# Kernel tuning notes

Measured on AMD Instinct MI355X. Metric: run time of the kernel, lower is better.

## Reference

```python
import jax, jax.numpy as jnp
import numpy as np


def setup_inputs() -> dict:
    key = jax.random.key(0)
    k1, k2 = jax.random.split(key)
    B, Nq, Nk, D = 8, 2048, 2048, 512
    query = jax.random.normal(k1, (B, Nq, D), dtype=jnp.float32)
    kv = jax.random.normal(k2, (B, Nk, D), dtype=jnp.float32)
    return {"query": query, "key": kv}


def reference(query, key):
    # Unscaled dot-product attention; value tensor is `key` itself.
    scores = jnp.einsum('bqd,bkd->bqk', query, key)  # [B, Nq, Nk]
    probs = jax.nn.softmax(scores, axis=-1)
    return jnp.einsum('bqk,bkd->bqd', probs, key)
```

## Files before the change

kernel.cpp:

```cpp
#include <hip/hip_runtime.h>

typedef _Float16 half8   __attribute__((ext_vector_type(8)));
typedef float    floatx4 __attribute__((ext_vector_type(4)));
typedef float    floatx16 __attribute__((ext_vector_type(16)));
typedef unsigned uintx2  __attribute__((ext_vector_type(2)));

#define LOG2E 1.44269504088896340736f

#define NQ  2048
#define NK  2048
#define DIM 512
#define KT  32
#define NTILES 64
#define IMG_BYTES 32768
#define WS_NEED ((size_t)8 * NTILES * IMG_BYTES)

#define PKRT(a,b) __builtin_bit_cast(unsigned, __builtin_amdgcn_cvt_pkrtz((a),(b)))


__global__ __launch_bounds__(256, 2)
void prep_k(const float* __restrict__ Kg, char* __restrict__ wsK)
{
    __shared__ __align__(16) _Float16 sImg[KT * DIM];
    const int tid = threadIdx.x;
    const int tileIdx = blockIdx.x;
    const int batch = tileIdx >> 6;
    const int kt    = tileIdx & 63;

    #pragma unroll
    for (int i = 0; i < 4; ++i) {
        const int idx = i * 256 + tid;
        const int k  = idx >> 5;
        const int db = idx & 31;
        const float* kp = Kg + ((size_t)batch * NK + (size_t)kt * KT + k) * DIM + db * 16;
        float4 f0 = *(const float4*)(kp + 0);
        float4 f1 = *(const float4*)(kp + 4);
        float4 f2 = *(const float4*)(kp + 8);
        float4 f3 = *(const float4*)(kp + 12);
        uint4 w0, w1;
        w0.x = PKRT(f0.x, f0.y); w0.y = PKRT(f0.z, f0.w);
        w0.z = PKRT(f1.x, f1.y); w0.w = PKRT(f1.z, f1.w);
        w1.x = PKRT(f2.x, f2.y); w1.y = PKRT(f2.z, f2.w);
        w1.z = PKRT(f3.x, f3.y); w1.w = PKRT(f3.z, f3.w);
        const int off = ((k >> 4) * 32 + db) * 256 + (k & 15) * 16;
        *(uint4*)&sImg[off + 0] = w0;
        *(uint4*)&sImg[off + 8] = w1;
    }
    __syncthreads();
    char* dst = wsK + (size_t)tileIdx * IMG_BYTES;
    const char* src = (const char*)sImg;
    #pragma unroll
    for (int i = 0; i < 8; ++i) {
        const int off = i * 4096 + tid * 16;
        *(uint4*)(dst + off) = *(const uint4*)(src + off);
    }
}

__device__ __forceinline__ void gld16(const char* g, char* l)
{
    __builtin_amdgcn_global_load_lds(
        (const __attribute__((address_space(1))) void*)g,
        (__attribute__((address_space(3))) void*)l, 16, 0, 0);
}

__global__ __launch_bounds__(512, 2)
void attn_fa3(const float* __restrict__ Qg, const char* __restrict__ wsK,
              float* __restrict__ Og)
{
    __shared__ __align__(16) char  sK[2][2][IMG_BYTES];
    __shared__ __align__(16) float sSx[8 * 64 * 8];

    const int tid  = threadIdx.x;
    const int lane = tid & 63;
    const int wave = tid >> 6;
    const int strip  = wave & 1;
    const int dh     = (wave >> 1) & 1;
    const int stream = wave >> 2;
    const int ql   = lane & 31;
    const int h    = lane >> 5;

    const int batch = blockIdx.x & 7;
    const int qtile = blockIdx.x >> 3;
    const int qrow  = qtile * 64 + strip * 32 + ql;
    const int dbase = dh * 256;

    const char* img = wsK + ((size_t)(batch * NTILES + stream * 32)) * IMG_BYTES;

    const float* qp = Qg + ((size_t)batch * NQ + qrow) * DIM + dbase + h * 8;
    half8 qf[16];
    #pragma unroll
    for (int dc = 0; dc < 16; ++dc) {
        float4 f0 = *(const float4*)(qp + dc * 16);
        float4 f1 = *(const float4*)(qp + dc * 16 + 4);
        union { unsigned u[4]; half8 hh; } t;
        t.u[0] = PKRT(f0.x, f0.y); t.u[1] = PKRT(f0.z, f0.w);
        t.u[2] = PKRT(f1.x, f1.y); t.u[3] = PKRT(f1.z, f1.w);
        qf[dc] = t.hh;
    }
    asm volatile("" ::: "memory");

    floatx16 acc[8];
    #pragma unroll
    for (int dt = 0; dt < 8; ++dt) {
        #pragma unroll
        for (int e = 0; e < 16; ++e) acc[dt][e] = 0.f;
    }
    float m_run = -INFINITY;
    float l_run = 0.f;

    const int laneA = ((lane >> 4) & 1) * 16384 + (lane & 15) * 32 + h * 16;
    const int laneT = ((lane >> 4) & 1) * 512 + h * 256 + (lane & 15) * 8;

    auto issue = [&](int t, int bi) {
        const char* src = img + (size_t)t * IMG_BYTES;
        char* dst = &sK[stream][bi][0];
        const int cw = (wave & 3) * 8;
        #pragma unroll
        for (int i = 0; i < 8; ++i) {
            const int c = cw + i;
            gld16(src + c * 1024 + lane * 16, dst + c * 1024);
        }
    };

    issue(0, 0);

    for (int kt = 0; kt < 32; ++kt) {
        const int bi = kt & 1;
        issue((kt + 1) & 31, bi ^ 1);

        asm volatile("s_waitcnt vmcnt(8)" ::: "memory");
        __builtin_amdgcn_s_barrier();
        __builtin_amdgcn_sched_barrier(0);

        const char* buf = &sK[stream][bi][0];

        union SS { floatx16 v; floatx4 q[4]; float f[16]; } s;
        {
            floatx16 sv;
            #pragma unroll
            for (int e = 0; e < 16; ++e) sv[e] = 0.f;
            const char* ap = buf + dh * 8192 + laneA;
            #pragma unroll
            for (int dc = 0; dc < 16; ++dc) {
                half8 a = *(const half8*)(ap + dc * 512);
                sv = __builtin_amdgcn_mfma_f32_32x32x16_f16(a, qf[dc], sv, 0, 0, 0);
            }
            s.v = sv;
        }

        float* slot  = &sSx[(wave * 64 + lane) * 8];
        const float* pslot = &sSx[((wave ^ 2) * 64 + lane) * 8];
        *(floatx4*)(slot + 0) = s.q[0];
        *(floatx4*)(slot + 4) = s.q[1];
        asm volatile("s_waitcnt lgkmcnt(0)" ::: "memory");
        __builtin_amdgcn_s_barrier();
        __builtin_amdgcn_sched_barrier(0);
        floatx4 r0 = *(const floatx4*)(pslot + 0);
        floatx4 r1 = *(const floatx4*)(pslot + 4);
        asm volatile("s_waitcnt lgkmcnt(0)" ::: "memory");
        __builtin_amdgcn_s_barrier();
        __builtin_amdgcn_sched_barrier(0);
        *(floatx4*)(slot + 0) = s.q[2];
        *(floatx4*)(slot + 4) = s.q[3];
        s.q[0] += r0; s.q[1] += r1;
        asm volatile("s_waitcnt lgkmcnt(0)" ::: "memory");
        __builtin_amdgcn_s_barrier();
        __builtin_amdgcn_sched_barrier(0);
        floatx4 r2 = *(const floatx4*)(pslot + 0);
        floatx4 r3 = *(const floatx4*)(pslot + 4);
        s.q[2] += r2; s.q[3] += r3;

        float mloc = s.f[0];
        #pragma unroll
        for (int r = 1; r < 16; ++r) mloc = fmaxf(mloc, s.f[r]);
        mloc = fmaxf(mloc, __shfl_xor(mloc, 32));
        const float m_new = fmaxf(m_run, mloc);
        const int grow = __any(mloc > m_run);

        float sl = 0.f;
        unsigned pk[8];
        #pragma unroll
        for (int s8 = 0; s8 < 8; ++s8) {
            const float pa = exp2f((s.f[2 * s8]     - m_new) * LOG2E);
            const float pb = exp2f((s.f[2 * s8 + 1] - m_new) * LOG2E);
            sl += pa + pb;
            pk[s8] = PKRT(pa, pb);
        }
        sl += __shfl_xor(sl, 32);
        if (grow) {
            const float alpha = exp2f((m_run - m_new) * LOG2E);
            l_run = l_run * alpha + sl;
            m_run = m_new;
            #pragma unroll
            for (int dt = 0; dt < 8; ++dt) acc[dt] *= alpha;
        } else {
            l_run += sl;
        }

        unsigned sw[8];
        #pragma unroll
        for (int s8 = 0; s8 < 8; ++s8)
            sw[s8] = (unsigned)__shfl_xor((int)pk[s8], 32);
        union PB { unsigned u[4]; half8 hh; } b0, b1;
        b0.u[0] = h ? sw[2] : pk[0];  b0.u[1] = h ? sw[3] : pk[1];
        b0.u[2] = h ? pk[2] : sw[0];  b0.u[3] = h ? pk[3] : sw[1];
        b1.u[0] = h ? sw[6] : pk[4];  b1.u[1] = h ? sw[7] : pk[5];
        b1.u[2] = h ? pk[6] : sw[4];  b1.u[3] = h ? pk[7] : sw[5];

        const unsigned bufA =
            (unsigned)(size_t)(__attribute__((address_space(3))) const char*)buf
            + (unsigned)(dh * 8192 + laneT);
        #pragma unroll
        for (int dt = 0; dt < 8; ++dt) {
            uintx2 t0, t1, t2, t3;
            const unsigned a0 = bufA + dt * 1024;
            const unsigned a1 = a0 + 16384;
            asm volatile(
                "ds_read_b64_tr_b16 %0, %4\n\t"
                "ds_read_b64_tr_b16 %1, %4 offset:128\n\t"
                "ds_read_b64_tr_b16 %2, %5\n\t"
                "ds_read_b64_tr_b16 %3, %5 offset:128"
                : "=&v"(t0), "=&v"(t1), "=&v"(t2), "=&v"(t3)
                : "v"(a0), "v"(a1));
            asm volatile("s_waitcnt lgkmcnt(0)" ::: "memory");
            __builtin_amdgcn_sched_barrier(0);
            union AF { uintx2 d[2]; half8 hh; } A0, A1;
            A0.d[0] = t0; A0.d[1] = t1;
            A1.d[0] = t2; A1.d[1] = t3;
            acc[dt] = __builtin_amdgcn_mfma_f32_32x32x16_f16(A0.hh, b0.hh, acc[dt], 0, 0, 0);
            acc[dt] = __builtin_amdgcn_mfma_f32_32x32x16_f16(A1.hh, b1.hh, acc[dt], 0, 0, 0);
        }

        __builtin_amdgcn_s_barrier();
        __builtin_amdgcn_sched_barrier(0);
    }

    {
        sSx[(wave * 64 + lane) * 2 + 0] = m_run;
        sSx[(wave * 64 + lane) * 2 + 1] = l_run;
        __syncthreads();
        const float pm = sSx[((wave ^ 4) * 64 + lane) * 2 + 0];
        const float pl = sSx[((wave ^ 4) * 64 + lane) * 2 + 1];
        const float mt   = fmaxf(m_run, pm);
        const float aown = exp2f((m_run - mt) * LOG2E);
        const float aoth = exp2f((pm   - mt) * LOG2E);
        const float lt   = l_run * aown + pl * aoth;
        const float inv  = 1.f / lt;
        (void)aoth;
        __syncthreads();

        float* op = Og + ((size_t)batch * NQ + qrow) * DIM + dbase;
        #pragma unroll
        for (int dt = 0; dt < 8; ++dt) {
            union SS2 { floatx16 v; floatx4 q[4]; } w;
            w.v = acc[dt] * aown;
            if (stream == 1) {
                float* sp = &sSx[(((wave & 3) * 64) + lane) * 16];
                *(floatx4*)(sp + 0)  = w.q[0];
                *(floatx4*)(sp + 4)  = w.q[1];
                *(floatx4*)(sp + 8)  = w.q[2];
                *(floatx4*)(sp + 12) = w.q[3];
            }
            __syncthreads();
            if (stream == 0) {
                const float* sp = &sSx[((wave * 64) + lane) * 16];
                #pragma unroll
                for (int g = 0; g < 4; ++g) {
                    floatx4 r = *(const floatx4*)(sp + g * 4);
                    floatx4 o = (w.q[g] + r) * inv;
                    *(floatx4*)(op + dt * 32 + g * 8 + 4 * h) = o;
                }
            }
            __syncthreads();
        }
    }
}

__global__ __launch_bounds__(256, 2)
void attn_fa(const float* __restrict__ Qg, const float* __restrict__ Kg,
             float* __restrict__ Og)
{
    __shared__ __align__(16) _Float16 sKr[KT * 512];
    __shared__ __align__(16) _Float16 sKt[256 * 72];
    __shared__ __align__(16) float    sSx[4 * 2 * 64 * 4];

    const int tid  = threadIdx.x;
    const int lane = tid & 63;
    const int wave = tid >> 6;
    const int quad = lane >> 4;
    const int col  = lane & 15;
    const int wq   = wave & 1;
    const int wg   = wave >> 1;
    const int dbase = wg * 256;

    const int batch = blockIdx.x & 7;
    const int qtile = blockIdx.x >> 3;
    const int qrow  = qtile * 32 + wq * 16 + col;

    const float* qp = Qg + ((size_t)batch * NQ + qrow) * DIM + dbase + quad * 8;
    half8 qf[8];
    #pragma unroll
    for (int dc = 0; dc < 8; ++dc) {
        float4 f0 = *(const float4*)(qp + dc * 32);
        float4 f1 = *(const float4*)(qp + dc * 32 + 4);
        union { unsigned u[4]; half8 hh; } t;
        t.u[0] = PKRT(f0.x, f0.y); t.u[1] = PKRT(f0.z, f0.w);
        t.u[2] = PKRT(f1.x, f1.y); t.u[3] = PKRT(f1.z, f1.w);
        qf[dc] = t.hh;
    }

    floatx4 acc[16];
    #pragma unroll
    for (int i = 0; i < 16; ++i) acc[i] = (floatx4){0.f, 0.f, 0.f, 0.f};

    float m_run = -INFINITY;
    float l_run = 0.f;
    const int keyc = ((col & 3) << 1) | ((col >> 2) & 1);

    for (int kt = 0; kt < NK / KT; ++kt) {
        __syncthreads();
        {
            const float* kp = Kg + ((size_t)batch * NK + kt * KT + wave * 8) * DIM + lane * 8;
            float rv[8][8];
            #pragma unroll
            for (int kk = 0; kk < 8; ++kk) {
                float4 f0 = *(const float4*)(kp + kk * DIM);
                float4 f1 = *(const float4*)(kp + kk * DIM + 4);
                rv[kk][0] = f0.x; rv[kk][1] = f0.y; rv[kk][2] = f0.z; rv[kk][3] = f0.w;
                rv[kk][4] = f1.x; rv[kk][5] = f1.y; rv[kk][6] = f1.z; rv[kk][7] = f1.w;
            }
            #pragma unroll
            for (int kk = 0; kk < 8; ++kk) {
                const int row = wave * 8 + kk;
                const int key = ((row & 3) << 1) | ((row >> 2) & 1);
                uint4 w;
                w.x = PKRT(rv[kk][0], rv[kk][1]); w.y = PKRT(rv[kk][2], rv[kk][3]);
                w.z = PKRT(rv[kk][4], rv[kk][5]); w.w = PKRT(rv[kk][6], rv[kk][7]);
                *(uint4*)&sKr[row * 512 + ((lane ^ key) << 3)] = w;
            }
            #pragma unroll
            for (int dd = 0; dd < 8; ++dd) {
                const int pp = dd >> 1;
                const int b  = dd & 1;
                const int slot = (pp << 6) | lane;
                uint4 w;
                w.x = PKRT(rv[0][dd], rv[1][dd]); w.y = PKRT(rv[2][dd], rv[3][dd]);
                w.z = PKRT(rv[4][dd], rv[5][dd]); w.w = PKRT(rv[6][dd], rv[7][dd]);
                *(uint4*)&sKt[slot * 72 + ((wave ^ pp) << 4) + (b << 3)] = w;
            }
        }
        __syncthreads();

        floatx4 s0 = {0.f, 0.f, 0.f, 0.f}, s1 = {0.f, 0.f, 0.f, 0.f};
        #pragma unroll
        for (int dc = 0; dc < 8; ++dc) {
            const int g = wg * 32 + dc * 4 + quad;
            const int off = ((g ^ keyc) << 3);
            half8 a0 = *(const half8*)&sKr[col * 512 + off];
            half8 a1 = *(const half8*)&sKr[(col + 16) * 512 + off];
            s0 = __builtin_amdgcn_mfma_f32_16x16x32_f16(a0, qf[dc], s0, 0, 0, 0);
            s1 = __builtin_amdgcn_mfma_f32_16x16x32_f16(a1, qf[dc], s1, 0, 0, 0);
        }

        *(floatx4*)&sSx[((wave * 2 + 0) * 64 + lane) * 4] = s0;
        *(floatx4*)&sSx[((wave * 2 + 1) * 64 + lane) * 4] = s1;
        __syncthreads();
        {
            const int pw = wave ^ 2;
            s0 += *(const floatx4*)&sSx[((pw * 2 + 0) * 64 + lane) * 4];
            s1 += *(const floatx4*)&sSx[((pw * 2 + 1) * 64 + lane) * 4];
        }

        float mloc = fmaxf(fmaxf(fmaxf(s0[0], s0[1]), fmaxf(s0[2], s0[3])),
                           fmaxf(fmaxf(s1[0], s1[1]), fmaxf(s1[2], s1[3])));
        mloc = fmaxf(mloc, __shfl_xor(mloc, 16));
        mloc = fmaxf(mloc, __shfl_xor(mloc, 32));
        const float m_new = fmaxf(m_run, mloc);
        const float alpha = exp2f((m_run - m_new) * LOG2E);
        const float p0 = exp2f((s0[0] - m_new) * LOG2E);
        const float p1 = exp2f((s0[1] - m_new) * LOG2E);
        const float p2 = exp2f((s0[2] - m_new) * LOG2E);
        const float p3 = exp2f((s0[3] - m_new) * LOG2E);
        const float p4 = exp2f((s1[0] - m_new) * LOG2E);
        const float p5 = exp2f((s1[1] - m_new) * LOG2E);
        const float p6 = exp2f((s1[2] - m_new) * LOG2E);
        const float p7 = exp2f((s1[3] - m_new) * LOG2E);
        float sloc = ((p0 + p1) + (p2 + p3)) + ((p4 + p5) + (p6 + p7));
        sloc += __shfl_xor(sloc, 16);
        sloc += __shfl_xor(sloc, 32);
        l_run = l_run * alpha + sloc;
        m_run = m_new;

        #pragma unroll
        for (int i = 0; i < 16; ++i) acc[i] *= alpha;

        const unsigned pk00 = PKRT(p0, p1);
        const unsigned pk01 = PKRT(p2, p3);
        const unsigned pk10 = PKRT(p4, p5);
        const unsigned pk11 = PKRT(p6, p7);
        const int srcA = col + ((quad & 1) << 5);
        const int srcB = srcA + 16;
        const unsigned a00 = (unsigned)__shfl((int)pk00, srcA);
        const unsigned a01 = (unsigned)__shfl((int)pk01, srcA);
        const unsigned a10 = (unsigned)__shfl((int)pk10, srcA);
        const unsigned a11 = (unsigned)__shfl((int)pk11, srcA);
        const unsigned b00 = (unsigned)__shfl((int)pk00, srcB);
        const unsigned b01 = (unsigned)__shfl((int)pk01, srcB);
        const unsigned b10 = (unsigned)__shfl((int)pk10, srcB);
        const unsigned b11 = (unsigned)__shfl((int)pk11, srcB);
        const bool hi2 = (quad >= 2);
        union { unsigned u[4]; half8 hh; } pt;
        pt.u[0] = hi2 ? a10 : a00;
        pt.u[1] = hi2 ? a11 : a01;
        pt.u[2] = hi2 ? b10 : b00;
        pt.u[3] = hi2 ? b11 : b01;
        const half8 pf = pt.hh;

        #pragma unroll
        for (int dt = 0; dt < 16; ++dt) {
            const int drow = dbase + dt * 16 + col;
            const int dp = drow >> 1;
            const int off = (((dp & 3) << 6) | (dp >> 2)) * 72
                          + ((quad ^ (dp & 3)) << 4) + ((drow & 1) << 3);
            half8 af = *(const half8*)&sKt[off];
            acc[dt] = __builtin_amdgcn_mfma_f32_16x16x32_f16(af, pf, acc[dt], 0, 0, 0);
        }
    }

    const float inv = 1.f / l_run;
    float* op = Og + ((size_t)batch * NQ + qrow) * DIM + dbase + quad * 4;
    #pragma unroll
    for (int dt = 0; dt < 16; ++dt) {
        floatx4 v = acc[dt] * inv;
        *(floatx4*)(op + dt * 16) = v;
    }
}

extern "C" void kernel_launch(void* const* d_in, const int* in_sizes, int n_in,
                              void* d_out, int out_size, void* d_ws, size_t ws_size,
                              hipStream_t stream) {
    (void)in_sizes; (void)n_in; (void)out_size;
    const float* Q = (const float*)d_in[0];
    const float* K = (const float*)d_in[1];
    float* O = (float*)d_out;
    if (d_ws != nullptr && ws_size >= WS_NEED) {
        char* wsK = (char*)d_ws;
        hipLaunchKernelGGL(prep_k,   dim3(8 * NTILES), dim3(256), 0, stream, K, wsK);
        hipLaunchKernelGGL(attn_fa3, dim3(256),        dim3(512), 0, stream, Q, wsK, O);
    } else {
        hipLaunchKernelGGL(attn_fa,  dim3(512),        dim3(256), 0, stream, Q, K, O);
    }
}
```

Before: 213.7 us.

## Cut barriers in score reduction, lazy rescale, setprio around MFMA, direct-store K prep

```diff
diff --git a/kernel.cpp b/kernel.cpp
--- a/kernel.cpp
+++ b/kernel.cpp
@@ -21,18 +21,22 @@
 __global__ __launch_bounds__(256, 2)
 void prep_k(const float* __restrict__ Kg, char* __restrict__ wsK)
 {
-    __shared__ __align__(16) _Float16 sImg[KT * DIM];
     const int tid = threadIdx.x;
     const int tileIdx = blockIdx.x;
     const int batch = tileIdx >> 6;
     const int kt    = tileIdx & 63;
 
+    char* img = wsK + (size_t)tileIdx * IMG_BYTES;
+    const float* base = Kg + ((size_t)batch * NK + (size_t)kt * KT) * DIM;
+
     #pragma unroll
     for (int i = 0; i < 4; ++i) {
         const int idx = i * 256 + tid;
-        const int k  = idx >> 5;
-        const int db = idx & 31;
-        const float* kp = Kg + ((size_t)batch * NK + (size_t)kt * KT + k) * DIM + db * 16;
+        const int kr  = idx & 15;
+        const int sub = idx >> 4;
+        const int kb  = sub >> 5;
+        const int db  = sub & 31;
+        const float* kp = base + (size_t)(kb * 16 + kr) * DIM + db * 16;
         float4 f0 = *(const float4*)(kp + 0);
         float4 f1 = *(const float4*)(kp + 4);
         float4 f2 = *(const float4*)(kp + 8);
@@ -42,17 +46,9 @@
         w0.z = PKRT(f1.x, f1.y); w0.w = PKRT(f1.z, f1.w);
         w1.x = PKRT(f2.x, f2.y); w1.y = PKRT(f2.z, f2.w);
         w1.z = PKRT(f3.x, f3.y); w1.w = PKRT(f3.z, f3.w);
-        const int off = ((k >> 4) * 32 + db) * 256 + (k & 15) * 16;
-        *(uint4*)&sImg[off + 0] = w0;
-        *(uint4*)&sImg[off + 8] = w1;
-    }
-    __syncthreads();
-    char* dst = wsK + (size_t)tileIdx * IMG_BYTES;
-    const char* src = (const char*)sImg;
-    #pragma unroll
-    for (int i = 0; i < 8; ++i) {
-        const int off = i * 4096 + tid * 16;
-        *(uint4*)(dst + off) = *(const uint4*)(src + off);
+        char* dst = img + sub * 512 + kr * 32;
+        *(uint4*)(dst + 0)  = w0;
+        *(uint4*)(dst + 16) = w1;
     }
 }
 
@@ -64,11 +60,11 @@
 }
 
 __global__ __launch_bounds__(512, 2)
-void attn_fa3(const float* __restrict__ Qg, const char* __restrict__ wsK,
+void attn_fa4(const float* __restrict__ Qg, const char* __restrict__ wsK,
               float* __restrict__ Og)
 {
     __shared__ __align__(16) char  sK[2][2][IMG_BYTES];
-    __shared__ __align__(16) float sSx[8 * 64 * 8];
+    __shared__ __align__(16) float sSx[8192];
 
     const int tid  = threadIdx.x;
     const int lane = tid & 63;
@@ -140,62 +136,58 @@
             #pragma unroll
             for (int e = 0; e < 16; ++e) sv[e] = 0.f;
             const char* ap = buf + dh * 8192 + laneA;
+            __builtin_amdgcn_s_setprio(1);
             #pragma unroll
             for (int dc = 0; dc < 16; ++dc) {
                 half8 a = *(const half8*)(ap + dc * 512);
                 sv = __builtin_amdgcn_mfma_f32_32x32x16_f16(a, qf[dc], sv, 0, 0, 0);
             }
+            __builtin_amdgcn_s_setprio(0);
             s.v = sv;
         }
 
-        float* slot  = &sSx[(wave * 64 + lane) * 8];
-        const float* pslot = &sSx[((wave ^ 2) * 64 + lane) * 8];
-        *(floatx4*)(slot + 0) = s.q[0];
-        *(floatx4*)(slot + 4) = s.q[1];
+        {
+            float* wp = sSx + wave * 1024 + lane * 4;
+            *(floatx4*)(wp + 0)   = s.q[0];
+            *(floatx4*)(wp + 256) = s.q[1];
+            *(floatx4*)(wp + 512) = s.q[2];
+            *(floatx4*)(wp + 768) = s.q[3];
+        }
         asm volatile("s_waitcnt lgkmcnt(0)" ::: "memory");
         __builtin_amdgcn_s_barrier();
         __builtin_amdgcn_sched_barrier(0);
-        floatx4 r0 = *(const floatx4*)(pslot + 0);
-        floatx4 r1 = *(const floatx4*)(pslot + 4);
-        asm volatile("s_waitcnt lgkmcnt(0)" ::: "memory");
-        __builtin_amdgcn_s_barrier();
-        __builtin_amdgcn_sched_barrier(0);
-        *(floatx4*)(slot + 0) = s.q[2];
-        *(floatx4*)(slot + 4) = s.q[3];
-        s.q[0] += r0; s.q[1] += r1;
-        asm volatile("s_waitcnt lgkmcnt(0)" ::: "memory");
-        __builtin_amdgcn_s_barrier();
-        __builtin_amdgcn_sched_barrier(0);
-        floatx4 r2 = *(const floatx4*)(pslot + 0);
-        floatx4 r3 = *(const floatx4*)(pslot + 4);
-        s.q[2] += r2; s.q[3] += r3;
+        {
+            const float* rp = sSx + (wave ^ 2) * 1024 + lane * 4;
+            s.q[0] += *(const floatx4*)(rp + 0);
+            s.q[1] += *(const floatx4*)(rp + 256);
+            s.q[2] += *(const floatx4*)(rp + 512);
+            s.q[3] += *(const floatx4*)(rp + 768);
+        }
 
         float mloc = s.f[0];
         #pragma unroll
         for (int r = 1; r < 16; ++r) mloc = fmaxf(mloc, s.f[r]);
         mloc = fmaxf(mloc, __shfl_xor(mloc, 32));
-        const float m_new = fmaxf(m_run, mloc);
-        const int grow = __any(mloc > m_run);
+        if (!__all(mloc <= m_run + 8.f)) {
+            const float m_new = fmaxf(m_run, mloc);
+            const float alpha = exp2f((m_run - m_new) * LOG2E);
+            l_run *= alpha;
+            #pragma unroll
+            for (int dt = 0; dt < 8; ++dt) acc[dt] *= alpha;
+            m_run = m_new;
+        }
 
         float sl = 0.f;
         unsigned pk[8];
         #pragma unroll
         for (int s8 = 0; s8 < 8; ++s8) {
-            const float pa = exp2f((s.f[2 * s8]     - m_new) * LOG2E);
-            const float pb = exp2f((s.f[2 * s8 + 1] - m_new) * LOG2E);
+            const float pa = exp2f((s.f[2 * s8]     - m_run) * LOG2E);
+            const float pb = exp2f((s.f[2 * s8 + 1] - m_run) * LOG2E);
             sl += pa + pb;
             pk[s8] = PKRT(pa, pb);
         }
         sl += __shfl_xor(sl, 32);
-        if (grow) {
-            const float alpha = exp2f((m_run - m_new) * LOG2E);
-            l_run = l_run * alpha + sl;
-            m_run = m_new;
-            #pragma unroll
-            for (int dt = 0; dt < 8; ++dt) acc[dt] *= alpha;
-        } else {
-            l_run += sl;
-        }
+        l_run += sl;
 
         unsigned sw[8];
         #pragma unroll
@@ -210,6 +202,7 @@
         const unsigned bufA =
             (unsigned)(size_t)(__attribute__((address_space(3))) const char*)buf
             + (unsigned)(dh * 8192 + laneT);
+        __builtin_amdgcn_s_setprio(1);
         #pragma unroll
         for (int dt = 0; dt < 8; ++dt) {
             uintx2 t0, t1, t2, t3;
@@ -230,6 +223,7 @@
             acc[dt] = __builtin_amdgcn_mfma_f32_32x32x16_f16(A0.hh, b0.hh, acc[dt], 0, 0, 0);
             acc[dt] = __builtin_amdgcn_mfma_f32_32x32x16_f16(A1.hh, b1.hh, acc[dt], 0, 0, 0);
         }
+        __builtin_amdgcn_s_setprio(0);
 
         __builtin_amdgcn_s_barrier();
         __builtin_amdgcn_sched_barrier(0);
@@ -446,7 +440,7 @@
     if (d_ws != nullptr && ws_size >= WS_NEED) {
         char* wsK = (char*)d_ws;
         hipLaunchKernelGGL(prep_k,   dim3(8 * NTILES), dim3(256), 0, stream, K, wsK);
-        hipLaunchKernelGGL(attn_fa3, dim3(256),        dim3(512), 0, stream, Q, wsK, O);
+        hipLaunchKernelGGL(attn_fa4, dim3(256),        dim3(512), 0, stream, Q, wsK, O);
     } else {
         hipLaunchKernelGGL(attn_fa,  dim3(512),        dim3(256), 0, stream, Q, K, O);
     }
```

New measurement: 205.9 us. 1.04x faster.
